# Kernel tuning notes

Hardware: AMD Instinct MI355X
Metric: run time of the kernel (lower is better)

## Reference

```python
import jax, jax.numpy as jnp
import numpy as np

DIM = 2048
NUM_HEADS = 16
HEAD_DIM = DIM // NUM_HEADS  # 128
HIDDEN = HEAD_DIM * NUM_HEADS  # 2048


def setup_inputs() -> dict:
    key = jax.random.key(0)
    k1, k2, k3 = jax.random.split(key, 3)
    x = jax.random.normal(k1, (2, 4096, DIM), dtype=jnp.float32)
    # match torch init: gates.weight ~ N(0, dim**-0.5), output.weight ~ N(0, hidden**-0.5)
    Wg = jax.random.normal(k2, (NUM_HEADS + 3 * HIDDEN, DIM), dtype=jnp.float32) * DIM ** -0.5
    bg = jnp.zeros((NUM_HEADS + 3 * HIDDEN,), dtype=jnp.float32)
    Wo = jax.random.normal(k3, (DIM, HIDDEN), dtype=jnp.float32) * HIDDEN ** -0.5
    bo = jnp.zeros((DIM,), dtype=jnp.float32)
    return {"x": x, "Wg": Wg, "bg": bg, "Wo": Wo, "bo": bo}


def _combine(a, b):
    # linear recurrence c_t = f_t * c_{t-1} + u_t as an associative op
    fa, ua = a
    fb, ub = b
    return fa * fb, fb * ua + ub


def reference(x, Wg, bg, Wo, bo):
    # x: [B, T, dim]
    g = jnp.einsum('btd,gd->btg', x, Wg) + bg  # [B, T, H + 3*hidden]
    f = jax.nn.sigmoid(g[..., :NUM_HEADS])  # [B, T, H]
    i = jax.nn.sigmoid(g[..., NUM_HEADS:NUM_HEADS + HIDDEN])
    t = jnp.tanh(g[..., NUM_HEADS + HIDDEN:NUM_HEADS + 2 * HIDDEN])
    o = g[..., NUM_HEADS + 2 * HIDDEN:]
    f = jnp.repeat(f, HEAD_DIM, axis=-1)  # tied forget gate per head -> [B, T, hidden]
    update = i * t
    # scan over time axis (axis=1)
    _, c = jax.lax.associative_scan(_combine, (f, update), axis=1)
    h = o * jnp.tanh(c)
    return jnp.einsum('bth,dh->btd', h, Wo) + bo
```

## Files before the change

### kernel.cpp

```cpp
#include <hip/hip_runtime.h>
#include <hip/hip_bf16.h>

#define DIM 2048
#define NHEADS 16
#define HEAD_DIM 128
#define HIDDEN 2048
#define SEQ 4096
#define BATCH 2
#define BT (BATCH * SEQ)
#define NSEG 64
#define SEGLEN (SEQ / NSEG)
#define N_GATE (3 * HIDDEN)

typedef __bf16 bf16_t;
typedef __bf16 bf16x8 __attribute__((ext_vector_type(8)));
typedef __bf16 bf16x4_t __attribute__((ext_vector_type(4)));
typedef float f32x4 __attribute__((ext_vector_type(4)));

__device__ __forceinline__ void gload_lds16(const void* g, void* l) {
  __builtin_amdgcn_global_load_lds(
      (const __attribute__((address_space(1))) void*)g,
      (__attribute__((address_space(3))) void*)l, 16, 0, 0);
}

#define MEMFENCE asm volatile("" ::: "memory")
#define BAR do { MEMFENCE; __builtin_amdgcn_s_barrier(); MEMFENCE; } while (0)
#define LGKM0 do { asm volatile("s_waitcnt lgkmcnt(0)" ::: "memory"); \
                   __builtin_amdgcn_sched_barrier(0); } while (0)
#define VMCNT(n) asm volatile("s_waitcnt vmcnt(" #n ")" ::: "memory")

__global__ void cvt_f32_bf16(const float* __restrict__ src, bf16_t* __restrict__ dst, int n4) {
  int i = blockIdx.x * blockDim.x + threadIdx.x;
  if (i >= n4) return;
  float4 v = reinterpret_cast<const float4*>(src)[i];
  bf16x4_t o;
  o[0] = (bf16_t)v.x; o[1] = (bf16_t)v.y; o[2] = (bf16_t)v.z; o[3] = (bf16_t)v.w;
  reinterpret_cast<bf16x4_t*>(dst)[i] = o;
}

__global__ void fgate_kernel(const float* __restrict__ x, const float* __restrict__ Wg,
                             const float* __restrict__ bg, float* __restrict__ fout) {
  int idx = blockIdx.x * 256 + threadIdx.x;
  int bt = idx >> 4, h = idx & 15;
  const float* xr = x + (size_t)bt * DIM;
  const float* wr = Wg + (size_t)h * DIM;
  float acc = 0.f;
  for (int k = 0; k < DIM; k += 4) {
    float4 xv = *reinterpret_cast<const float4*>(xr + k);
    float4 wv = *reinterpret_cast<const float4*>(wr + k);
    acc = fmaf(xv.x, wv.x, acc);
    acc = fmaf(xv.y, wv.y, acc);
    acc = fmaf(xv.z, wv.z, acc);
    acc = fmaf(xv.w, wv.w, acc);
  }
  acc += bg[h];
  fout[idx] = 1.f / (1.f + expf(-acc));
}


__device__ __forceinline__ void stage_unit(const bf16_t* __restrict__ G, int grow0, int kcol,
                                           bf16_t* region, int j, int wid, int lane) {
  const int r = j * 64 + wid * 8 + (lane >> 3);
  const int c = (lane & 7) ^ (lane >> 3);
  gload_lds16(G + (size_t)(grow0 + r) * 2048 + kcol + c * 8,
              region + (size_t)(j * 64 + wid * 8) * 64);
}

#define FRAG8(ptr, row, fo) (*reinterpret_cast<const bf16x8*>(&(ptr)[(size_t)(row) * 64 + (fo)]))

template <int MODE>
__global__ __launch_bounds__(512, 1)
void gemm256(const bf16_t* __restrict__ A, const bf16_t* __restrict__ B,
             const float* __restrict__ bias,
             bf16_t* __restrict__ Oi, bf16_t* __restrict__ Ot, bf16_t* __restrict__ Oo,
             float* __restrict__ Of, int tiles_n) {
  __shared__ __align__(16) bf16_t As[2][2][128 * 64];
  __shared__ __align__(16) bf16_t Bs[2][2][128 * 64];
  constexpr int KT = 32;

  const int tid = threadIdx.x;
  const int wid = tid >> 6, lane = tid & 63;
  const int nwg = gridDim.x, bid = blockIdx.x;
  const int swz = (bid & 7) * (nwg >> 3) + (bid >> 3);
  const int tm = swz / tiles_n, tn = swz - tm * tiles_n;
  const int brow = tm * 256, bcol = tn * 256;
  const int wm = wid >> 2, wn = wid & 3;
  const int rl = lane & 15, q = lane >> 4;
  const int cx = rl & 7;
  const int fo0 = ((q ^ cx) << 3);
  const int fo1 = fo0 ^ 32;
  const int bnh = wn >> 1, brl = (wn & 1) * 64;

  f32x4 acc[8][4] = {};

  stage_unit(B, bcol,       0, &Bs[0][0][0], 0, wid, lane);
  stage_unit(B, bcol,       0, &Bs[0][0][0], 1, wid, lane);
  stage_unit(B, bcol + 128, 0, &Bs[0][1][0], 0, wid, lane);
  stage_unit(B, bcol + 128, 0, &Bs[0][1][0], 1, wid, lane);
  stage_unit(A, brow,       0, &As[0][0][0], 0, wid, lane);
  stage_unit(A, brow + 128, 0, &As[0][1][0], 0, wid, lane);
  stage_unit(A, brow,       0, &As[0][0][0], 1, wid, lane);
  stage_unit(A, brow + 128, 0, &As[0][1][0], 1, wid, lane);

  for (int t = 0; t < KT; ++t) {
    const int s = t & 1, ns = s ^ 1;
    const bool s1 = (t + 1) < KT;
    const int kc1 = (t + 1) * 64;
    const bf16_t* a = &As[s][wm][0];
    const bf16_t* b = &Bs[s][bnh][0];
    bf16x8 af[4], bf[4];

    VMCNT(2);
    BAR;
    if (s1) { stage_unit(B, bcol,       kc1, &Bs[ns][0][0], 0, wid, lane);
              stage_unit(B, bcol,       kc1, &Bs[ns][0][0], 1, wid, lane); }
#pragma unroll
    for (int ni = 0; ni < 4; ++ni) bf[ni] = FRAG8(b, brl + ni * 16 + rl, fo0);
#pragma unroll
    for (int m = 0; m < 4; ++m)    af[m]  = FRAG8(a, m * 16 + rl, fo0);
    LGKM0;
    __builtin_amdgcn_s_setprio(1);
#pragma unroll
    for (int m = 0; m < 4; ++m)
#pragma unroll
      for (int ni = 0; ni < 4; ++ni)
        acc[m][ni] = __builtin_amdgcn_mfma_f32_16x16x32_bf16(af[m], bf[ni], acc[m][ni], 0, 0, 0);
    __builtin_amdgcn_s_setprio(0);

    if (s1) { VMCNT(2); } else { VMCNT(0); }
    BAR;
    if (s1) { stage_unit(B, bcol + 128, kc1, &Bs[ns][1][0], 0, wid, lane);
              stage_unit(B, bcol + 128, kc1, &Bs[ns][1][0], 1, wid, lane); }
#pragma unroll
    for (int m = 0; m < 4; ++m) af[m] = FRAG8(a, 64 + m * 16 + rl, fo0);
    LGKM0;
    __builtin_amdgcn_s_setprio(1);
#pragma unroll
    for (int m = 0; m < 4; ++m)
#pragma unroll
      for (int ni = 0; ni < 4; ++ni)
        acc[4 + m][ni] = __builtin_amdgcn_mfma_f32_16x16x32_bf16(af[m], bf[ni], acc[4 + m][ni], 0, 0, 0);
    __builtin_amdgcn_s_setprio(0);

    if (s1) { stage_unit(A, brow,       kc1, &As[ns][0][0], 0, wid, lane);
              stage_unit(A, brow + 128, kc1, &As[ns][1][0], 0, wid, lane); }
#pragma unroll
    for (int ni = 0; ni < 4; ++ni) bf[ni] = FRAG8(b, brl + ni * 16 + rl, fo1);
#pragma unroll
    for (int m = 0; m < 4; ++m)    af[m]  = FRAG8(a, m * 16 + rl, fo1);
    LGKM0;
    __builtin_amdgcn_s_setprio(1);
#pragma unroll
    for (int m = 0; m < 4; ++m)
#pragma unroll
      for (int ni = 0; ni < 4; ++ni)
        acc[m][ni] = __builtin_amdgcn_mfma_f32_16x16x32_bf16(af[m], bf[ni], acc[m][ni], 0, 0, 0);
    __builtin_amdgcn_s_setprio(0);

    if (s1) { stage_unit(A, brow,       kc1, &As[ns][0][0], 1, wid, lane);
              stage_unit(A, brow + 128, kc1, &As[ns][1][0], 1, wid, lane); }
#pragma unroll
    for (int m = 0; m < 4; ++m) af[m] = FRAG8(a, 64 + m * 16 + rl, fo1);
    LGKM0;
    __builtin_amdgcn_s_setprio(1);
#pragma unroll
    for (int m = 0; m < 4; ++m)
#pragma unroll
      for (int ni = 0; ni < 4; ++ni)
        acc[4 + m][ni] = __builtin_amdgcn_mfma_f32_16x16x32_bf16(af[m], bf[ni], acc[4 + m][ni], 0, 0, 0);
    __builtin_amdgcn_s_setprio(0);
  }

  const int crow0 = brow + wm * 128;
  const int ccol0 = bcol + wn * 64;
  if (MODE == 0) {
    const int section = bcol >> 11;
    bf16_t* dst = (section == 0) ? Oi : ((section == 1) ? Ot : Oo);
#pragma unroll
    for (int mi = 0; mi < 8; ++mi)
#pragma unroll
      for (int ni = 0; ni < 4; ++ni) {
        int gcol = ccol0 + ni * 16 + (lane & 15);
        int col = gcol & 2047;
        float bv = bias[gcol];
#pragma unroll
        for (int qq = 0; qq < 4; ++qq) {
          int row = crow0 + mi * 16 + (lane >> 4) * 4 + qq;
          float v = acc[mi][ni][qq] + bv;
          float aout;
          if (section == 0)      aout = 1.f / (1.f + __expf(-v));
          else if (section == 1) aout = tanhf(v);
          else                   aout = v;
          dst[(size_t)row * HIDDEN + col] = (bf16_t)aout;
        }
      }
  } else {
#pragma unroll
    for (int mi = 0; mi < 8; ++mi)
#pragma unroll
      for (int ni = 0; ni < 4; ++ni) {
        int col = ccol0 + ni * 16 + (lane & 15);
        float bv = bias[col];
#pragma unroll
        for (int qq = 0; qq < 4; ++qq) {
          int row = crow0 + mi * 16 + (lane >> 4) * 4 + qq;
          Of[(size_t)row * DIM + col] = acc[mi][ni][qq] + bv;
        }
      }
  }
}

__global__ void scan_pass1(const float* __restrict__ fg, const bf16_t* __restrict__ gi,
                           const bf16_t* __restrict__ gt, float* __restrict__ cend,
                           float* __restrict__ pseg) {
  int bx = blockIdx.x;
  int chblk = bx & 7, seg = (bx >> 3) & 63, b = bx >> 9;
  int ch = chblk * 256 + threadIdx.x;
  int head = ch >> 7;
  float c = 0.f, P = 1.f;
  size_t t0 = (size_t)b * SEQ + (size_t)seg * SEGLEN;
  for (int tt = 0; tt < SEGLEN; ++tt) {
    size_t bt = t0 + tt;
    float f = fg[bt * NHEADS + head];
    float iv = (float)gi[bt * HIDDEN + ch];
    float tv = (float)gt[bt * HIDDEN + ch];
    c = fmaf(f, c, iv * tv);
    P *= f;
  }
  size_t o = ((size_t)b * NSEG + seg) * HIDDEN + ch;
  cend[o] = c;
  pseg[o] = P;
}

__global__ void scan_pass2(const float* __restrict__ cend, const float* __restrict__ pseg,
                           float* __restrict__ cin) {
  int idx = blockIdx.x * 256 + threadIdx.x;
  int b = idx >> 11, ch = idx & 2047;
  float C = 0.f;
  for (int s = 0; s < NSEG; ++s) {
    size_t o = ((size_t)b * NSEG + s) * HIDDEN + ch;
    cin[o] = C;
    C = cend[o] + pseg[o] * C;
  }
}

__global__ void scan_pass3(const float* __restrict__ fg, const bf16_t* __restrict__ gi,
                           const bf16_t* __restrict__ gt, const bf16_t* __restrict__ go,
                           const float* __restrict__ cin, bf16_t* __restrict__ h) {
  int bx = blockIdx.x;
  int chblk = bx & 7, seg = (bx >> 3) & 63, b = bx >> 9;
  int ch = chblk * 256 + threadIdx.x;
  int head = ch >> 7;
  float c = cin[((size_t)b * NSEG + seg) * HIDDEN + ch];
  size_t t0 = (size_t)b * SEQ + (size_t)seg * SEGLEN;
  for (int tt = 0; tt < SEGLEN; ++tt) {
    size_t bt = t0 + tt;
    float f = fg[bt * NHEADS + head];
    float iv = (float)gi[bt * HIDDEN + ch];
    float tv = (float)gt[bt * HIDDEN + ch];
    c = fmaf(f, c, iv * tv);
    float hv = (float)go[bt * HIDDEN + ch] * tanhf(c);
    h[bt * HIDDEN + ch] = (bf16_t)hv;
  }
}

extern "C" void kernel_launch(void* const* d_in, const int* in_sizes, int n_in,
                              void* d_out, int out_size, void* d_ws, size_t ws_size,
                              hipStream_t stream) {
  const float* x  = (const float*)d_in[0];
  const float* Wg = (const float*)d_in[1];
  const float* bg = (const float*)d_in[2];
  const float* Wo = (const float*)d_in[3];
  const float* bo = (const float*)d_in[4];
  float* out = (float*)d_out;

  char* ws = (char*)d_ws;
  size_t off = 0;
  auto alloc = [&](size_t bytes) -> void* {
    void* p = ws + off;
    off += (bytes + 255) & ~(size_t)255;
    return p;
  };
  bf16_t* xb   = (bf16_t*)alloc((size_t)BT * DIM * 2);
  bf16_t* wgb  = (bf16_t*)alloc((size_t)N_GATE * DIM * 2);
  bf16_t* wob  = (bf16_t*)alloc((size_t)DIM * HIDDEN * 2);
  float*  fg   = (float*)alloc((size_t)BT * NHEADS * 4);
  bf16_t* gi   = (bf16_t*)alloc((size_t)BT * HIDDEN * 2);
  bf16_t* gt   = (bf16_t*)alloc((size_t)BT * HIDDEN * 2);
  bf16_t* go   = (bf16_t*)alloc((size_t)BT * HIDDEN * 2);
  bf16_t* hbuf = (bf16_t*)alloc((size_t)BT * HIDDEN * 2);
  float*  cend = (float*)alloc((size_t)BATCH * NSEG * HIDDEN * 4);
  float*  pseg = (float*)alloc((size_t)BATCH * NSEG * HIDDEN * 4);
  float*  cin  = (float*)alloc((size_t)BATCH * NSEG * HIDDEN * 4);
  (void)ws_size; (void)in_sizes; (void)n_in; (void)out_size;

  {
    int n4 = BT * DIM / 4;
    cvt_f32_bf16<<<(n4 + 255) / 256, 256, 0, stream>>>(x, xb, n4);
  }
  {
    int n4 = N_GATE * DIM / 4;
    cvt_f32_bf16<<<(n4 + 255) / 256, 256, 0, stream>>>(Wg + (size_t)NHEADS * DIM, wgb, n4);
  }
  {
    int n4 = DIM * HIDDEN / 4;
    cvt_f32_bf16<<<(n4 + 255) / 256, 256, 0, stream>>>(Wo, wob, n4);
  }

  fgate_kernel<<<(BT * NHEADS) / 256, 256, 0, stream>>>(x, Wg, bg, fg);

  gemm256<0><<<768, 512, 0, stream>>>(xb, wgb, bg + NHEADS, gi, gt, go, nullptr, 24);

  scan_pass1<<<BATCH * NSEG * (HIDDEN / 256), 256, 0, stream>>>(fg, gi, gt, cend, pseg);
  scan_pass2<<<BATCH * HIDDEN / 256, 256, 0, stream>>>(cend, pseg, cin);
  scan_pass3<<<BATCH * NSEG * (HIDDEN / 256), 256, 0, stream>>>(fg, gi, gt, go, cin, hbuf);

  gemm256<1><<<256, 512, 0, stream>>>(hbuf, wob, bo, nullptr, nullptr, nullptr, out, 8);
}
```

Measured before the change: 610.2 us.

## Restructure GEMM mainloop with quarter-row A staging and deeper prefetch

Reorganises the LDS layout so A is staged in 64-row quarters with a permuted row mapping, and A quarters for k-tile t+2 are prefetched into the buffer being consumed once each quarter has been read. B fragments for both k-halves are loaded once per k-tile and reused across four MFMA phases, which cuts redundant LDS reads. The goal is deeper global-to-LDS overlap and fewer fragment loads. The cost is more barriers per iteration and intricate vmcnt accounting that could stall or race.

```diff
diff --git a/kernel.cpp b/kernel.cpp
--- a/kernel.cpp
+++ b/kernel.cpp
@@ -58,12 +58,20 @@
 }
 
 
-__device__ __forceinline__ void stage_unit(const bf16_t* __restrict__ G, int grow0, int kcol,
-                                           bf16_t* region, int j, int wid, int lane) {
-  const int r = j * 64 + wid * 8 + (lane >> 3);
-  const int c = (lane & 7) ^ (lane >> 3);
-  gload_lds16(G + (size_t)(grow0 + r) * 2048 + kcol + c * 8,
-              region + (size_t)(j * 64 + wid * 8) * 64);
+__device__ __forceinline__ void stageA(const bf16_t* __restrict__ G, int brow, int kc,
+                                       bf16_t* Aslot, int q, int wid, int lane) {
+  const int rr = q * 64 + wid * 8;
+  const int grow = brow + (wid >> 2) * 128 + q * 32 + (wid & 3) * 8 + (lane >> 3);
+  const int gcol = kc + (((lane & 7) ^ (lane >> 3)) << 3);
+  gload_lds16(G + (size_t)grow * 2048 + gcol, Aslot + (size_t)rr * 64);
+}
+
+__device__ __forceinline__ void stageB(const bf16_t* __restrict__ G, int bcol, int kc,
+                                       bf16_t* Bslot, int j, int wid, int lane) {
+  const int rr = (j >> 1) * 128 + (j & 1) * 64 + wid * 8;
+  const int grow = bcol + rr + (lane >> 3);
+  const int gcol = kc + (((lane & 7) ^ (lane >> 3)) << 3);
+  gload_lds16(G + (size_t)grow * 2048 + gcol, Bslot + (size_t)rr * 64);
 }
 
 #define FRAG8(ptr, row, fo) (*reinterpret_cast<const bf16x8*>(&(ptr)[(size_t)(row) * 64 + (fo)]))
@@ -74,8 +82,8 @@
              const float* __restrict__ bias,
              bf16_t* __restrict__ Oi, bf16_t* __restrict__ Ot, bf16_t* __restrict__ Oo,
              float* __restrict__ Of, int tiles_n) {
-  __shared__ __align__(16) bf16_t As[2][2][128 * 64];
-  __shared__ __align__(16) bf16_t Bs[2][2][128 * 64];
+  __shared__ __align__(16) bf16_t As[2][256 * 64];
+  __shared__ __align__(16) bf16_t Bs[2][256 * 64];
   constexpr int KT = 32;
 
   const int tid = threadIdx.x;
@@ -85,90 +93,99 @@
   const int tm = swz / tiles_n, tn = swz - tm * tiles_n;
   const int brow = tm * 256, bcol = tn * 256;
   const int wm = wid >> 2, wn = wid & 3;
-  const int rl = lane & 15, q = lane >> 4;
-  const int cx = rl & 7;
-  const int fo0 = ((q ^ cx) << 3);
+  const int rl = lane & 15, qw = lane >> 4;
+  const int fo0 = ((qw ^ (rl & 7)) << 3);
   const int fo1 = fo0 ^ 32;
-  const int bnh = wn >> 1, brl = (wn & 1) * 64;
+  const int brr = (wn >> 1) * 128 + (wn & 1) * 64;
 
   f32x4 acc[8][4] = {};
 
-  stage_unit(B, bcol,       0, &Bs[0][0][0], 0, wid, lane);
-  stage_unit(B, bcol,       0, &Bs[0][0][0], 1, wid, lane);
-  stage_unit(B, bcol + 128, 0, &Bs[0][1][0], 0, wid, lane);
-  stage_unit(B, bcol + 128, 0, &Bs[0][1][0], 1, wid, lane);
-  stage_unit(A, brow,       0, &As[0][0][0], 0, wid, lane);
-  stage_unit(A, brow + 128, 0, &As[0][1][0], 0, wid, lane);
-  stage_unit(A, brow,       0, &As[0][0][0], 1, wid, lane);
-  stage_unit(A, brow + 128, 0, &As[0][1][0], 1, wid, lane);
+#pragma unroll
+  for (int j = 0; j < 4; ++j) stageB(B, bcol, 0, &Bs[0][0], j, wid, lane);
+#pragma unroll
+  for (int qq = 0; qq < 4; ++qq) stageA(A, brow, 0, &As[0][0], qq, wid, lane);
+#pragma unroll
+  for (int qq = 0; qq < 3; ++qq) stageA(A, brow, 64, &As[1][0], qq, wid, lane);
+  VMCNT(3);
+  BAR;
 
   for (int t = 0; t < KT; ++t) {
     const int s = t & 1, ns = s ^ 1;
-    const bool s1 = (t + 1) < KT;
-    const int kc1 = (t + 1) * 64;
-    const bf16_t* a = &As[s][wm][0];
-    const bf16_t* b = &Bs[s][bnh][0];
-    bf16x8 af[4], bf[4];
-
-    VMCNT(2);
+    const int kc1 = (t + 1) * 64, kc2 = (t + 2) * 64;
+    const bool st1 = (t + 1) < KT, st2 = (t + 2) < KT;
+    const bf16_t* Ar = &As[s][0];
+    const bf16_t* Br = &Bs[s][0];
+    bf16x8 bfr[2][4], af[2][2];
+
+#define MFMA16(p)                                                                         \
+  __builtin_amdgcn_s_setprio(1);                                                          \
+  _Pragma("unroll")                                                                       \
+  for (int mi = 0; mi < 2; ++mi)                                                          \
+    _Pragma("unroll")                                                                     \
+    for (int ni = 0; ni < 4; ++ni)                                                        \
+      acc[(p)*2 + mi][ni] =                                                               \
+          __builtin_amdgcn_mfma_f32_16x16x32_bf16(af[0][mi], bfr[0][ni], acc[(p)*2 + mi][ni], 0, 0, 0); \
+  _Pragma("unroll")                                                                       \
+  for (int mi = 0; mi < 2; ++mi)                                                          \
+    _Pragma("unroll")                                                                     \
+    for (int ni = 0; ni < 4; ++ni)                                                        \
+      acc[(p)*2 + mi][ni] =                                                               \
+          __builtin_amdgcn_mfma_f32_16x16x32_bf16(af[1][mi], bfr[1][ni], acc[(p)*2 + mi][ni], 0, 0, 0); \
+  __builtin_amdgcn_s_setprio(0)
+
+#pragma unroll
+    for (int ni = 0; ni < 4; ++ni) {
+      bfr[0][ni] = FRAG8(Br, brr + ni * 16 + rl, fo0);
+      bfr[1][ni] = FRAG8(Br, brr + ni * 16 + rl, fo1);
+    }
+#pragma unroll
+    for (int mi = 0; mi < 2; ++mi) {
+      af[0][mi] = FRAG8(Ar, 0 * 64 + wm * 32 + mi * 16 + rl, fo0);
+      af[1][mi] = FRAG8(Ar, 0 * 64 + wm * 32 + mi * 16 + rl, fo1);
+    }
+    if (st1) { stageB(B, bcol, kc1, &Bs[ns][0], 0, wid, lane);
+               stageB(B, bcol, kc1, &Bs[ns][0], 1, wid, lane); }
+    asm volatile("s_waitcnt lgkmcnt(8)" ::: "memory");
+    BAR; LGKM0;
+    MFMA16(0);
     BAR;
-    if (s1) { stage_unit(B, bcol,       kc1, &Bs[ns][0][0], 0, wid, lane);
-              stage_unit(B, bcol,       kc1, &Bs[ns][0][0], 1, wid, lane); }
-#pragma unroll
-    for (int ni = 0; ni < 4; ++ni) bf[ni] = FRAG8(b, brl + ni * 16 + rl, fo0);
-#pragma unroll
-    for (int m = 0; m < 4; ++m)    af[m]  = FRAG8(a, m * 16 + rl, fo0);
-    LGKM0;
-    __builtin_amdgcn_s_setprio(1);
-#pragma unroll
-    for (int m = 0; m < 4; ++m)
-#pragma unroll
-      for (int ni = 0; ni < 4; ++ni)
-        acc[m][ni] = __builtin_amdgcn_mfma_f32_16x16x32_bf16(af[m], bf[ni], acc[m][ni], 0, 0, 0);
-    __builtin_amdgcn_s_setprio(0);
-
-    if (s1) { VMCNT(2); } else { VMCNT(0); }
+
+#pragma unroll
+    for (int mi = 0; mi < 2; ++mi) {
+      af[0][mi] = FRAG8(Ar, 1 * 64 + wm * 32 + mi * 16 + rl, fo0);
+      af[1][mi] = FRAG8(Ar, 1 * 64 + wm * 32 + mi * 16 + rl, fo1);
+    }
+    if (st1) { stageB(B, bcol, kc1, &Bs[ns][0], 2, wid, lane);
+               stageB(B, bcol, kc1, &Bs[ns][0], 3, wid, lane); }
+    if (t < KT - 1) { VMCNT(4); } else { VMCNT(0); }
+    BAR; LGKM0;
+    MFMA16(1);
     BAR;
-    if (s1) { stage_unit(B, bcol + 128, kc1, &Bs[ns][1][0], 0, wid, lane);
-              stage_unit(B, bcol + 128, kc1, &Bs[ns][1][0], 1, wid, lane); }
-#pragma unroll
-    for (int m = 0; m < 4; ++m) af[m] = FRAG8(a, 64 + m * 16 + rl, fo0);
-    LGKM0;
-    __builtin_amdgcn_s_setprio(1);
-#pragma unroll
-    for (int m = 0; m < 4; ++m)
-#pragma unroll
-      for (int ni = 0; ni < 4; ++ni)
-        acc[4 + m][ni] = __builtin_amdgcn_mfma_f32_16x16x32_bf16(af[m], bf[ni], acc[4 + m][ni], 0, 0, 0);
-    __builtin_amdgcn_s_setprio(0);
-
-    if (s1) { stage_unit(A, brow,       kc1, &As[ns][0][0], 0, wid, lane);
-              stage_unit(A, brow + 128, kc1, &As[ns][1][0], 0, wid, lane); }
-#pragma unroll
-    for (int ni = 0; ni < 4; ++ni) bf[ni] = FRAG8(b, brl + ni * 16 + rl, fo1);
-#pragma unroll
-    for (int m = 0; m < 4; ++m)    af[m]  = FRAG8(a, m * 16 + rl, fo1);
-    LGKM0;
-    __builtin_amdgcn_s_setprio(1);
-#pragma unroll
-    for (int m = 0; m < 4; ++m)
-#pragma unroll
-      for (int ni = 0; ni < 4; ++ni)
-        acc[m][ni] = __builtin_amdgcn_mfma_f32_16x16x32_bf16(af[m], bf[ni], acc[m][ni], 0, 0, 0);
-    __builtin_amdgcn_s_setprio(0);
-
-    if (s1) { stage_unit(A, brow,       kc1, &As[ns][0][0], 1, wid, lane);
-              stage_unit(A, brow + 128, kc1, &As[ns][1][0], 1, wid, lane); }
-#pragma unroll
-    for (int m = 0; m < 4; ++m) af[m] = FRAG8(a, 64 + m * 16 + rl, fo1);
-    LGKM0;
-    __builtin_amdgcn_s_setprio(1);
-#pragma unroll
-    for (int m = 0; m < 4; ++m)
-#pragma unroll
-      for (int ni = 0; ni < 4; ++ni)
-        acc[4 + m][ni] = __builtin_amdgcn_mfma_f32_16x16x32_bf16(af[m], bf[ni], acc[4 + m][ni], 0, 0, 0);
-    __builtin_amdgcn_s_setprio(0);
+
+#pragma unroll
+    for (int mi = 0; mi < 2; ++mi) {
+      af[0][mi] = FRAG8(Ar, 2 * 64 + wm * 32 + mi * 16 + rl, fo0);
+      af[1][mi] = FRAG8(Ar, 2 * 64 + wm * 32 + mi * 16 + rl, fo1);
+    }
+    if (st2) { stageA(A, brow, kc2, &As[s][0], 0, wid, lane);
+               stageA(A, brow, kc2, &As[s][0], 1, wid, lane); }
+    BAR; LGKM0;
+    MFMA16(2);
+    BAR;
+
+#pragma unroll
+    for (int mi = 0; mi < 2; ++mi) {
+      af[0][mi] = FRAG8(Ar, 3 * 64 + wm * 32 + mi * 16 + rl, fo0);
+      af[1][mi] = FRAG8(Ar, 3 * 64 + wm * 32 + mi * 16 + rl, fo1);
+    }
+    if (st2) stageA(A, brow, kc2, &As[s][0], 2, wid, lane);
+    if (st1) stageA(A, brow, kc1, &As[ns][0], 3, wid, lane);
+    if (t < KT - 2) { VMCNT(4); }
+    else if (t == KT - 2) { VMCNT(1); }
+    BAR; LGKM0;
+    MFMA16(3);
+    BAR;
+#undef MFMA16
   }
 
   const int crow0 = brow + wm * 128;
```

After: 511.1 us. -16.2%, faster.
